# Kernel tuning notes

Hardware: AMD Instinct MI355X
Metric: run time of the kernel (lower is better)

## Reference

```python
import jax, jax.numpy as jnp
import numpy as np
from jax import lax

N, E, T, D = 50000, 400000, 16, 240
HID = 16  # LSTM hidden


def _p(k, shape):
    fan_in = shape[0]
    return jax.random.normal(k, shape, dtype=jnp.float32) * (1.0 / np.sqrt(fan_in))


def setup_inputs() -> dict:
    key = jax.random.key(0)
    ks = jax.random.split(key, 32)
    inp = {
        "x": jax.random.normal(ks[0], (N, D), dtype=jnp.float32),
        "edge_seq": jax.random.normal(ks[1], (E, T, 2), dtype=jnp.float32),
        "node_seq": jax.random.normal(ks[2], (N, T, 2), dtype=jnp.float32),
        # LSTM (torch gate order i,f,g,o); same lstm_edge is used for both edge and node seqs (as in source)
        "lstm_Wih": _p(ks[3], (4 * HID, 2)),
        "lstm_Whh": _p(ks[4], (4 * HID, HID)),
        "lstm_b": jnp.zeros((4 * HID,), jnp.float32),
        "dnn_W": _p(ks[5], (HID, 1)),
        "dnn_b": jnp.zeros((1,), jnp.float32),
        # gat1: in=256, heads=8, out=8 ; gat2: in=64, heads=1, out=64
        "gat1_W": _p(ks[6], (256, 64)),
        "gat1_att": _p(ks[7], (8, 8)),
        "gat1_b": jnp.zeros((64,), jnp.float32),
        "gat2_W": _p(ks[8], (64, 64)),
        "gat2_att": _p(ks[9], (1, 64)),
        "gat2_b": jnp.zeros((64,), jnp.float32),
        "gcn1_W": _p(ks[10], (256, 64)),
        "gcn1_b": jnp.zeros((64,), jnp.float32),
        "gcn2_W": _p(ks[11], (64, 64)),
        "gcn2_b": jnp.zeros((64,), jnp.float32),
        "cls1_W": _p(ks[12], (320, 32)),
        "cls1_b": jnp.zeros((32,), jnp.float32),
        "cls2_W": _p(ks[13], (32, 16)),
        "cls2_b": jnp.zeros((16,), jnp.float32),
        "cls3_W": _p(ks[14], (16, 4)),
        "cls3_b": jnp.zeros((4,), jnp.float32),
        "edge_index": jax.random.randint(ks[15], (2, E), 0, N),
        "edge_len": jax.random.randint(ks[16], (E,), 1, T + 1).astype(jnp.int32),
        "node_len": jax.random.randint(ks[17], (N,), 1, T + 1).astype(jnp.int32),
    }
    return inp


def lstm_last(seq, lens, Wih, Whh, b):
    """Run LSTM over padded [B,T,2] and return hidden at step len-1 (pack/pad_packed semantics)."""
    B, Tt, _ = seq.shape
    H = Whh.shape[1]

    def step(carry, inp):
        h, c, last = carry
        xt, t = inp
        g = xt @ Wih.T + h @ Whh.T + b
        i, f, gg, o = jnp.split(g, 4, axis=-1)
        c = jax.nn.sigmoid(f) * c + jax.nn.sigmoid(i) * jnp.tanh(gg)
        h = jax.nn.sigmoid(o) * jnp.tanh(c)
        last = jnp.where((t == lens - 1)[:, None], h, last)
        return (h, c, last), None

    z = jnp.zeros((B, H), seq.dtype)
    (_, _, last), _ = lax.scan(step, (z, z, z), (jnp.swapaxes(seq, 0, 1), jnp.arange(Tt)))
    return last


def gat_conv(x, src, dst, edge_scalar, W, att, bias, H, C):
    """myGATConv: gather -> leaky_relu -> softmax over dst neighborhoods -> (alpha + edge_mat)*x_j -> scatter-add + residual."""
    n = x.shape[0]
    xh = (x @ W).reshape(n, H, C)                       # [N,H,C]
    alpha = (xh * att[None]).sum(-1)                    # [N,H]
    a = jax.nn.leaky_relu(alpha[src], 0.2)              # [E,H] (alpha_j)
    amax = jax.ops.segment_max(a, dst, num_segments=n)
    ex = jnp.exp(a - amax[dst])
    att_e = ex / jax.ops.segment_sum(ex, dst, num_segments=n)[dst]
    coef = att_e + edge_scalar                          # [E,H] + [E,1] edge bias (edge_mat repeat over heads)
    msg = xh[src] * coef[..., None]                     # [E,H,C]
    out = jax.ops.segment_sum(msg, dst, num_segments=n) + xh  # aggregate + residual
    return out.reshape(n, H * C) + bias


def gcn_conv(x, src, dst, W, b):
    n = x.shape[0]
    xw = x @ W
    deg = jax.ops.segment_sum(jnp.ones(src.shape[0], xw.dtype), dst, num_segments=n) + 1.0  # +self-loop
    dinv = lax.rsqrt(deg)
    norm = (dinv[src] * dinv[dst])[:, None]
    out = jax.ops.segment_sum(xw[src] * norm, dst, num_segments=n) + xw * (dinv * dinv)[:, None]
    return out + b


def reference(x, edge_seq, node_seq, lstm_Wih, lstm_Whh, lstm_b, dnn_W, dnn_b,
              gat1_W, gat1_att, gat1_b, gat2_W, gat2_att, gat2_b,
              gcn1_W, gcn1_b, gcn2_W, gcn2_b,
              cls1_W, cls1_b, cls2_W, cls2_b, cls3_W, cls3_b,
              edge_index, edge_len, node_len):
    src, dst = edge_index[0], edge_index[1]
    # temporal edge branch -> per-edge scalar bias
    edge_feat = lstm_last(edge_seq, edge_len, lstm_Wih, lstm_Whh, lstm_b)   # [E,16]
    edge_scalar = edge_feat @ dnn_W + dnn_b                                 # [E,1]
    # temporal node branch (source reuses lstm_edge) -> concat to node features
    node_feat = lstm_last(node_seq, node_len, lstm_Wih, lstm_Whh, lstm_b)   # [N,16]
    xin = jnp.concatenate([x, node_feat], axis=-1)                          # [N,256]
    # GAT stack (no dropout: eval mode)
    x_gat = gat_conv(xin, src, dst, edge_scalar, gat1_W, gat1_att, gat1_b, 8, 8)
    x_gat = gat_conv(x_gat, src, dst, edge_scalar, gat2_W, gat2_att, gat2_b, 1, 64)
    x_gat = jnp.where(jnp.isinf(x_gat) | jnp.isnan(x_gat), 0.0, x_gat)
    lr = lambda v: jax.nn.leaky_relu(v, 0.01)
    # GCN stack (eval: dropout off)
    x_gcn = lr(gcn_conv(xin, src, dst, gcn1_W, gcn1_b))
    x_gcn = lr(gcn_conv(x_gcn, src, dst, gcn2_W, gcn2_b))
    # classifier head
    h = jnp.concatenate([xin, x_gcn], axis=1)
    h = lr(h @ cls1_W + cls1_b)
    h = lr(h @ cls2_W + cls2_b)
    out = h @ cls3_W + cls3_b
    return (out, x_gcn, x_gat)
```

## Files before the change

kernel.cpp:

```cpp
#include <hip/hip_runtime.h>
#include <hip/hip_bf16.h>


typedef unsigned int u32;

#define NN 50000
#define EE 400000

__device__ float g_nodeF[NN * 16];
__device__ float g_esc[EE];
__device__ float g_P1[NN * 64];
__device__ float g_P2[NN * 64];
__device__ float g_P3[NN * 64];
__device__ float g_P4[NN * 64];
__device__ float g_alpha[NN * 8];
__device__ float g_dinv[NN];
__device__ int   g_cnt[NN];
__device__ int   g_rs[NN + 1];
__device__ int   g_cur[NN];
__device__ int   g_csrc[EE];
__device__ float g_cesc[EE];
__device__ int   g_bhist[32];
__device__ int   g_bbase[32];
__device__ int   g_permN[NN];
__device__ int   g_permE[EE];
__device__ int   g_bsum[256];

__device__ __forceinline__ float rcpf(float x) { return __builtin_amdgcn_rcpf(x); }
__device__ __forceinline__ float ex2(float x)  { return __builtin_amdgcn_exp2f(x); }
__device__ __forceinline__ float sigf(float x) { return rcpf(1.0f + __expf(-x)); }

typedef short short8 __attribute__((ext_vector_type(8)));
typedef float f32x16 __attribute__((ext_vector_type(16)));

union S8U { short8 v; unsigned u[4]; };

__device__ __forceinline__ unsigned pk_hi(float a, float b) {
    return (__float_as_uint(a) >> 16) | (__float_as_uint(b) & 0xFFFF0000u);
}
__device__ __forceinline__ float bftrunc(float a) {
    return __uint_as_float(__float_as_uint(a) & 0xFFFF0000u);
}
__device__ __forceinline__ float lo_res(float a) { return a - bftrunc(a); }
__device__ __forceinline__ unsigned sx32(unsigned v) {
    return (unsigned)__shfl_xor((int)v, 32, 64);
}

__global__ void __launch_bounds__(256) bucket_hist_kernel(
    const int* __restrict__ nlen, const int* __restrict__ elen,
    const int* __restrict__ dstp, int* __restrict__ cnt)
{
    __shared__ int hb[32];
    int t = threadIdx.x;
    if (t < 32) hb[t] = 0;
    __syncthreads();
    int i = blockIdx.x * 256 + t;
    int bin = -1;
    if (i < NN + EE) {
        bin = (i < NN) ? (16 - nlen[i]) : (32 - elen[i - NN]);
    }
    if (bin >= 0) atomicAdd(&hb[bin], 1);
    if (i < EE) atomicAdd(&cnt[dstp[i]], 1);
    __syncthreads();
    if (t < 32 && hb[t] > 0) atomicAdd(&g_bhist[t], hb[t]);
}

__global__ void __launch_bounds__(64) bucket_scan_kernel()
{
    if (threadIdx.x == 0) {
        int acc = 0;
        for (int b = 0; b < 16; ++b) { g_bbase[b] = acc; acc += g_bhist[b]; }
        acc = 0;
        for (int b = 16; b < 32; ++b) { g_bbase[b] = acc; acc += g_bhist[b]; }
    }
}

__global__ void __launch_bounds__(256) bucket_scatter_kernel(
    const int* __restrict__ nlen, const int* __restrict__ elen)
{
    __shared__ int hb[32];
    int t = threadIdx.x;
    if (t < 32) hb[t] = 0;
    __syncthreads();
    int i = blockIdx.x * 256 + t;
    int bin = -1, idx = 0;
    if (i < NN + EE) {
        if (i < NN) { idx = i; bin = 16 - nlen[i]; }
        else        { idx = i - NN; bin = 32 - elen[i - NN]; }
    }
    if (bin >= 0) atomicAdd(&hb[bin], 1);
    __syncthreads();
    if (t < 32) {
        int c = hb[t];
        hb[t] = c > 0 ? atomicAdd(&g_bbase[t], c) : 0;
    }
    __syncthreads();
    if (bin >= 0) {
        int pos = atomicAdd(&hb[bin], 1);
        if (i < NN) g_permN[pos] = idx; else g_permE[pos] = idx;
    }
}

__global__ void __launch_bounds__(256, 3) lstm_fused_kernel(
    const float* __restrict__ nseq, const int* __restrict__ nlen,
    const float* __restrict__ eseq, const int* __restrict__ elen,
    const float* __restrict__ Wih, const float* __restrict__ Whh,
    const float* __restrict__ bias,
    const float* __restrict__ dnnW, const float* __restrict__ dnnb,
    const int* __restrict__ permN, const int* __restrict__ permE,
    float* __restrict__ nodeF, float* __restrict__ esc, int nNodeBlk)
{
    const int lane = threadIdx.x & 63;
    const int col  = lane & 31;
    const int hi   = lane >> 5;
    const bool isLo = (hi == 0);
    const int wave = threadIdx.x >> 6;

    const bool edgeMode = (int)blockIdx.x >= nNodeBlk;
    const float* seq = edgeMode ? eseq : nseq;
    const int*  lens = edgeMode ? elen : nlen;
    const int*  perm = edgeMode ? permE : permN;
    const int limit  = edgeMode ? EE : NN;
    const int bbase  = edgeMode ? ((int)blockIdx.x - nNodeBlk) : (int)blockIdx.x;
    const int g  = bbase * 128 + wave * 32 + col;
    const int gc = g < limit ? g : limit - 1;
    const int s  = perm[gc];
    const bool valid = g < limit;

    const float LOG2E = 1.44269504f;
    const int row0 = col, row1 = col + 32;
    const float s0 = LOG2E;
    const float s1 = (row1 < 48) ? 2.0f * LOG2E : LOG2E;
    const int ko = hi * 8;
    S8U ahh0, ahh1, ahl0, ahl1, ax0, ax1;
    {
        const float* w0 = Whh + row0 * 16 + ko;
        const float* w1 = Whh + row1 * 16 + ko;
#pragma unroll
        for (int r = 0; r < 4; ++r) {
            float a0 = w0[2 * r] * s0, b0 = w0[2 * r + 1] * s0;
            float a1 = w1[2 * r] * s1, b1 = w1[2 * r + 1] * s1;
            ahh0.u[r] = pk_hi(a0, b0);
            ahh1.u[r] = pk_hi(a1, b1);
            ahl0.u[r] = pk_hi(lo_res(a0), lo_res(b0));
            ahl1.u[r] = pk_hi(lo_res(a1), lo_res(b1));
        }
#pragma unroll
        for (int r = 0; r < 4; ++r) { ax0.u[r] = 0u; ax1.u[r] = 0u; }
        if (isLo) {
            float wa0 = Wih[row0 * 2] * s0, wb0 = Wih[row0 * 2 + 1] * s0, bb0 = bias[row0] * s0;
            float wa1 = Wih[row1 * 2] * s1, wb1 = Wih[row1 * 2 + 1] * s1, bb1 = bias[row1] * s1;
            ax0.u[0] = pk_hi(wa0, wb0);
            ax0.u[1] = pk_hi(bb0, wa0);
            ax0.u[2] = pk_hi(wb0, lo_res(wa0));
            ax0.u[3] = pk_hi(lo_res(wb0), lo_res(bb0));
            ax1.u[0] = pk_hi(wa1, wb1);
            ax1.u[1] = pk_hi(bb1, wa1);
            ax1.u[2] = pk_hi(wb1, lo_res(wa1));
            ax1.u[3] = pk_hi(lo_res(wb1), lo_res(bb1));
        }
    }

    const f32x16 zc = {0.f, 0.f, 0.f, 0.f, 0.f, 0.f, 0.f, 0.f,
                       0.f, 0.f, 0.f, 0.f, 0.f, 0.f, 0.f, 0.f};
    const unsigned bxmask = isLo ? 0xFFFFFFFFu : 0u;
    const unsigned one_bf = 0x3F80u;

    float cst[8], hlast[8];
#pragma unroll
    for (int j = 0; j < 8; ++j) { cst[j] = 0.f; hlast[j] = 0.f; }
    unsigned ph[4], pl[4];
#pragma unroll
    for (int r = 0; r < 4; ++r) { ph[r] = 0u; pl[r] = 0u; }

    const float4* sp = (const float4*)seq + (size_t)s * 8;
    const int lenm1 = lens[s] - 1;
    int lm = lenm1;
#pragma unroll
    for (int off = 32; off >= 1; off >>= 1) {
        int o = __shfl_xor(lm, off, 64);
        lm = lm > o ? lm : o;
    }
    const int nIter = (lm >> 1) + 1;

    float4 q = sp[0];
#pragma unroll 1
    for (int i = 0; i < nIter; ++i) {
        float4 qn = sp[(i + 1) & 7];
#pragma unroll
        for (int hf = 0; hf < 2; ++hf) {
            const int t = 2 * i + hf;
            const float x0 = hf ? q.z : q.x;
            const float x1 = hf ? q.w : q.y;

            S8U bhh, bhl, bx;
            {
                unsigned t0 = sx32(ph[0]), t1 = sx32(ph[1]);
                unsigned t2 = sx32(ph[2]), t3 = sx32(ph[3]);
                bhh.u[0] = isLo ? ph[0] : t2;
                bhh.u[1] = isLo ? ph[1] : t3;
                bhh.u[2] = isLo ? t0 : ph[2];
                bhh.u[3] = isLo ? t1 : ph[3];
                unsigned s0u = sx32(pl[0]), s1u = sx32(pl[1]);
                unsigned s2u = sx32(pl[2]), s3u = sx32(pl[3]);
                bhl.u[0] = isLo ? pl[0] : s2u;
                bhl.u[1] = isLo ? pl[1] : s3u;
                bhl.u[2] = isLo ? s0u : pl[2];
                bhl.u[3] = isLo ? s1u : pl[3];
            }
            {
                float xl0 = lo_res(x0), xl1 = lo_res(x1);
                bx.u[0] = pk_hi(x0, x1) & bxmask;
                bx.u[1] = (one_bf | (__float_as_uint(xl0) & 0xFFFF0000u)) & bxmask;
                bx.u[2] = pk_hi(xl1, x0) & bxmask;
                bx.u[3] = ((__float_as_uint(x1) >> 16) | (one_bf << 16)) & bxmask;
            }

            f32x16 d0 = __builtin_amdgcn_mfma_f32_32x32x16_bf16(ax0.v, bx.v, zc, 0, 0, 0);
            f32x16 d1 = __builtin_amdgcn_mfma_f32_32x32x16_bf16(ax1.v, bx.v, zc, 0, 0, 0);
            d0 = __builtin_amdgcn_mfma_f32_32x32x16_bf16(ahh0.v, bhh.v, d0, 0, 0, 0);
            d1 = __builtin_amdgcn_mfma_f32_32x32x16_bf16(ahh1.v, bhh.v, d1, 0, 0, 0);
            d0 = __builtin_amdgcn_mfma_f32_32x32x16_bf16(ahl0.v, bhh.v, d0, 0, 0, 0);
            d1 = __builtin_amdgcn_mfma_f32_32x32x16_bf16(ahl1.v, bhh.v, d1, 0, 0, 0);
            d0 = __builtin_amdgcn_mfma_f32_32x32x16_bf16(ahh0.v, bhl.v, d0, 0, 0, 0);
            d1 = __builtin_amdgcn_mfma_f32_32x32x16_bf16(ahh1.v, bhl.v, d1, 0, 0, 0);

            float hh[8];
#pragma unroll
            for (int j = 0; j < 8; ++j) {
                float ip = d0[j], fp = d0[8 + j], gp = d1[j], op = d1[8 + j];
                float sig_i = rcpf(1.0f + ex2(-ip));
                float sig_f = rcpf(1.0f + ex2(-fp));
                float th_g  = 1.0f - 2.0f * rcpf(ex2(gp) + 1.0f);
                float cu = sig_f * cst[j] + sig_i * th_g;
                cst[j] = cu;
                float th_c = 1.0f - 2.0f * rcpf(ex2(cu * 2.88539008f) + 1.0f);
                hh[j] = rcpf(1.0f + ex2(-op)) * th_c;
            }
            const bool selm = (t == lenm1);
#pragma unroll
            for (int j = 0; j < 8; ++j) hlast[j] = selm ? hh[j] : hlast[j];
#pragma unroll
            for (int r = 0; r < 4; ++r) {
                float a = hh[2 * r], b = hh[2 * r + 1];
                ph[r] = pk_hi(a, b);
                pl[r] = pk_hi(lo_res(a), lo_res(b));
            }
        }
        q = qn;
    }

    if (edgeMode) {
        float4 dA = *(const float4*)(dnnW + hi * 4);
        float4 dB = *(const float4*)(dnnW + hi * 4 + 8);
        float part = hlast[0] * dA.x + hlast[1] * dA.y + hlast[2] * dA.z + hlast[3] * dA.w
                   + hlast[4] * dB.x + hlast[5] * dB.y + hlast[6] * dB.z + hlast[7] * dB.w;
        float tot = part + __shfl_xor(part, 32, 64);
        if (isLo && valid) esc[s] = tot + dnnb[0];
    } else {
        if (valid) {
            float* dst = nodeF + (size_t)s * 16 + hi * 4;
            *(float4*)(dst)     = make_float4(hlast[0], hlast[1], hlast[2], hlast[3]);
            *(float4*)(dst + 8) = make_float4(hlast[4], hlast[5], hlast[6], hlast[7]);
        }
    }
}

__global__ void __launch_bounds__(256) zero_cnt_kernel(int* cnt, int n)
{
    int t = blockIdx.x * 256 + threadIdx.x;
    if (t < n) cnt[t] = 0;
    if (blockIdx.x == 0 && threadIdx.x < 32) g_bhist[threadIdx.x] = 0;
}

__global__ void __launch_bounds__(256) scan1_kernel(const int* __restrict__ cnt, int n)
{
    __shared__ int s[256];
    int t = threadIdx.x;
    int i = blockIdx.x * 256 + t;
    s[t] = (i < n) ? cnt[i] : 0;
    __syncthreads();
#pragma unroll
    for (int off = 128; off >= 1; off >>= 1) {
        if (t < off) s[t] += s[t + off];
        __syncthreads();
    }
    if (t == 0) g_bsum[blockIdx.x] = s[0];
}

__global__ void __launch_bounds__(256) scan3_kernel(
    const int* __restrict__ cnt, int* __restrict__ rs, int* __restrict__ cur,
    float* __restrict__ dinv, int n, int E, int nb)
{
    __shared__ int sb[256];
    __shared__ int s[256];
    int t = threadIdx.x;
    sb[t] = (t < nb) ? g_bsum[t] : 0;
    __syncthreads();
#pragma unroll
    for (int off = 1; off < 256; off <<= 1) {
        int add = (t >= off) ? sb[t - off] : 0;
        __syncthreads();
        sb[t] += add;
        __syncthreads();
    }
    const int boff = (blockIdx.x == 0) ? 0 : sb[blockIdx.x - 1];

    int i = blockIdx.x * 256 + t;
    int v = (i < n) ? cnt[i] : 0;
    s[t] = v;
    __syncthreads();
#pragma unroll
    for (int off = 1; off < 256; off <<= 1) {
        int add = (t >= off) ? s[t - off] : 0;
        __syncthreads();
        s[t] += add;
        __syncthreads();
    }
    if (i < n) {
        int excl = s[t] - v + boff;
        rs[i] = excl;
        cur[i] = excl;
        dinv[i] = rsqrtf((float)v + 1.0f);
    }
    if (i == 0) rs[n] = E;
}

__global__ void __launch_bounds__(256) fill_kernel(const int* __restrict__ src,
                                                   const int* __restrict__ dst,
                                                   const float* __restrict__ esc,
                                                   int* __restrict__ cur,
                                                   int* __restrict__ csrc,
                                                   float* __restrict__ cesc, int E)
{
    int e = blockIdx.x * 256 + threadIdx.x;
    if (e >= E) return;
    int pos = atomicAdd(&cur[dst[e]], 1);
    csrc[pos] = src[e];
    cesc[pos] = esc[e];
}

__global__ void __launch_bounds__(256, 2) gemmX_dual_kernel(
    const float* __restrict__ x, const float* __restrict__ nodeF,
    const float* __restrict__ Wg, const float* __restrict__ Wc,
    const float* __restrict__ att,
    float* __restrict__ Pg, float* __restrict__ Pc,
    float* __restrict__ alpha, int n)
{
    __shared__ unsigned sW[2][2][64 * 64];
    const int tid = threadIdx.x;
    const int lane = tid & 63;
    const int col  = lane & 31;
    const int hi   = lane >> 5;
    const int wv   = tid >> 6;
    const int nodeBase = blockIdx.x * 128 + wv * 32;
    const int nodeL = nodeBase + col;
    const int nc = nodeL < n ? nodeL : n - 1;
    const float* xrow = x + (size_t)nc * 240;
    const float* frow = nodeF + (size_t)nc * 16;
    const float attv0 = att[col];
    const float attv1 = att[32 + col];

    const f32x16 zc = {0.f, 0.f, 0.f, 0.f, 0.f, 0.f, 0.f, 0.f,
                       0.f, 0.f, 0.f, 0.f, 0.f, 0.f, 0.f, 0.f};
    f32x16 ag0 = zc, ag1 = zc, ac0 = zc, ac1 = zc;

#pragma unroll 1
    for (int p = 0; p < 2; ++p) {
        if (p) __syncthreads();
        for (int i = tid; i < 2 * 64 * 64; i += 256) {
            const int mat = i >> 12;
            const int jj  = i & 4095;
            const int kk2 = jj >> 6, c = jj & 63;
            const float* W = mat ? Wc : Wg;
            float a = W[(p * 64 + kk2) * 128 + c];
            float b = W[(p * 64 + kk2) * 128 + 64 + c];
            sW[mat][0][jj] = pk_hi(a, b);
            sW[mat][1][jj] = pk_hi(lo_res(a), lo_res(b));
        }
        __syncthreads();
#pragma unroll 1
        for (int ch = 0; ch < 8; ++ch) {
            const int gch = p * 8 + ch;
            const float* src = (gch < 15) ? (xrow + gch * 16 + hi * 8) : (frow + hi * 8);
            float4 v0 = *(const float4*)src;
            float4 v1 = *(const float4*)(src + 4);
            S8U xh, xl;
            xh.u[0] = pk_hi(v0.x, v0.y);
            xh.u[1] = pk_hi(v0.z, v0.w);
            xh.u[2] = pk_hi(v1.x, v1.y);
            xh.u[3] = pk_hi(v1.z, v1.w);
            xl.u[0] = pk_hi(lo_res(v0.x), lo_res(v0.y));
            xl.u[1] = pk_hi(lo_res(v0.z), lo_res(v0.w));
            xl.u[2] = pk_hi(lo_res(v1.x), lo_res(v1.y));
            xl.u[3] = pk_hi(lo_res(v1.z), lo_res(v1.w));

            const int rbase = (ch * 8 + hi * 4) * 64 + col;
            S8U gh0, gl0, gh1, gl1, ch0, cl0, ch1, cl1;
#pragma unroll
            for (int r = 0; r < 4; ++r) {
                gh0.u[r] = sW[0][0][rbase + r * 64];
                gl0.u[r] = sW[0][1][rbase + r * 64];
                gh1.u[r] = sW[0][0][rbase + r * 64 + 32];
                gl1.u[r] = sW[0][1][rbase + r * 64 + 32];
                ch0.u[r] = sW[1][0][rbase + r * 64];
                cl0.u[r] = sW[1][1][rbase + r * 64];
                ch1.u[r] = sW[1][0][rbase + r * 64 + 32];
                cl1.u[r] = sW[1][1][rbase + r * 64 + 32];
            }
            ag0 = __builtin_amdgcn_mfma_f32_32x32x16_bf16(xh.v, gh0.v, ag0, 0, 0, 0);
            ag1 = __builtin_amdgcn_mfma_f32_32x32x16_bf16(xh.v, gh1.v, ag1, 0, 0, 0);
            ag0 = __builtin_amdgcn_mfma_f32_32x32x16_bf16(xl.v, gh0.v, ag0, 0, 0, 0);
            ag1 = __builtin_amdgcn_mfma_f32_32x32x16_bf16(xl.v, gh1.v, ag1, 0, 0, 0);
            ag0 = __builtin_amdgcn_mfma_f32_32x32x16_bf16(xh.v, gl0.v, ag0, 0, 0, 0);
            ag1 = __builtin_amdgcn_mfma_f32_32x32x16_bf16(xh.v, gl1.v, ag1, 0, 0, 0);
            ac0 = __builtin_amdgcn_mfma_f32_32x32x16_bf16(xh.v, ch0.v, ac0, 0, 0, 0);
            ac1 = __builtin_amdgcn_mfma_f32_32x32x16_bf16(xh.v, ch1.v, ac1, 0, 0, 0);
            ac0 = __builtin_amdgcn_mfma_f32_32x32x16_bf16(xl.v, ch0.v, ac0, 0, 0, 0);
            ac1 = __builtin_amdgcn_mfma_f32_32x32x16_bf16(xl.v, ch1.v, ac1, 0, 0, 0);
            ac0 = __builtin_amdgcn_mfma_f32_32x32x16_bf16(xh.v, cl0.v, ac0, 0, 0, 0);
            ac1 = __builtin_amdgcn_mfma_f32_32x32x16_bf16(xh.v, cl1.v, ac1, 0, 0, 0);
        }
    }

#pragma unroll
    for (int r = 0; r < 16; ++r) {
        const int nr = (r & 3) + 8 * (r >> 2) + 4 * hi;
        const int nd = nodeBase + nr;
        const bool ok = nd < n;
        if (ok) {
            Pg[(size_t)nd * 64 + col]      = ag0[r];
            Pg[(size_t)nd * 64 + 32 + col] = ag1[r];
            Pc[(size_t)nd * 64 + col]      = ac0[r];
            Pc[(size_t)nd * 64 + 32 + col] = ac1[r];
        }
        float p0 = ag0[r] * attv0;
        float p1 = ag1[r] * attv1;
        p0 += __shfl_xor(p0, 1, 64); p0 += __shfl_xor(p0, 2, 64); p0 += __shfl_xor(p0, 4, 64);
        p1 += __shfl_xor(p1, 1, 64); p1 += __shfl_xor(p1, 2, 64); p1 += __shfl_xor(p1, 4, 64);
        if (ok && (col & 7) == 0) {
            alpha[(size_t)nd * 8 + (col >> 3)]     = p0;
            alpha[(size_t)nd * 8 + 4 + (col >> 3)] = p1;
        }
    }
}

__global__ void __launch_bounds__(256, 2) gemm64_dual_kernel(
    const float* __restrict__ Ag, const float* __restrict__ Ac,
    const float* __restrict__ Wg, const float* __restrict__ Wc,
    const float* __restrict__ att,
    float* __restrict__ Pg, float* __restrict__ Pc,
    float* __restrict__ alpha, int n)
{
    __shared__ unsigned sW[2][2][32 * 64];
    const int tid = threadIdx.x;
    for (int i = tid; i < 2 * 32 * 64; i += 256) {
        const int mat = i >> 11;
        const int jj  = i & 2047;
        const int kk2 = jj >> 6, c = jj & 63;
        const float* W = mat ? Wc : Wg;
        float a = W[kk2 * 128 + c];
        float b = W[kk2 * 128 + 64 + c];
        sW[mat][0][jj] = pk_hi(a, b);
        sW[mat][1][jj] = pk_hi(lo_res(a), lo_res(b));
    }
    __syncthreads();

    const int lane = tid & 63;
    const int col  = lane & 31;
    const int hi   = lane >> 5;
    const int wv   = tid >> 6;
    const int nodeBase = blockIdx.x * 128 + wv * 32;
    const int nodeL = nodeBase + col;
    const int nc = nodeL < n ? nodeL : n - 1;
    const float attv0 = att[col];
    const float attv1 = att[32 + col];

    const f32x16 zc = {0.f, 0.f, 0.f, 0.f, 0.f, 0.f, 0.f, 0.f,
                       0.f, 0.f, 0.f, 0.f, 0.f, 0.f, 0.f, 0.f};
    f32x16 bg0 = zc, bg1 = zc, bc0 = zc, bc1 = zc;

    const float* garow = Ag + (size_t)nc * 64;
    const float* carow = Ac + (size_t)nc * 64;
#pragma unroll
    for (int ch = 0; ch < 4; ++ch) {
        const int rbase = (ch * 8 + hi * 4) * 64 + col;
        S8U wh0, wl0, wh1, wl1;
        {
            const float* src = garow + ch * 16 + hi * 8;
            float4 v0 = *(const float4*)src;
            float4 v1 = *(const float4*)(src + 4);
            S8U xh, xl;
            xh.u[0] = pk_hi(v0.x, v0.y);
            xh.u[1] = pk_hi(v0.z, v0.w);
            xh.u[2] = pk_hi(v1.x, v1.y);
            xh.u[3] = pk_hi(v1.z, v1.w);
            xl.u[0] = pk_hi(lo_res(v0.x), lo_res(v0.y));
            xl.u[1] = pk_hi(lo_res(v0.z), lo_res(v0.w));
            xl.u[2] = pk_hi(lo_res(v1.x), lo_res(v1.y));
            xl.u[3] = pk_hi(lo_res(v1.z), lo_res(v1.w));
#pragma unroll
            for (int r = 0; r < 4; ++r) {
                wh0.u[r] = sW[0][0][rbase + r * 64];
                wl0.u[r] = sW[0][1][rbase + r * 64];
                wh1.u[r] = sW[0][0][rbase + r * 64 + 32];
                wl1.u[r] = sW[0][1][rbase + r * 64 + 32];
            }
            bg0 = __builtin_amdgcn_mfma_f32_32x32x16_bf16(xh.v, wh0.v, bg0, 0, 0, 0);
            bg1 = __builtin_amdgcn_mfma_f32_32x32x16_bf16(xh.v, wh1.v, bg1, 0, 0, 0);
            bg0 = __builtin_amdgcn_mfma_f32_32x32x16_bf16(xl.v, wh0.v, bg0, 0, 0, 0);
            bg1 = __builtin_amdgcn_mfma_f32_32x32x16_bf16(xl.v, wh1.v, bg1, 0, 0, 0);
            bg0 = __builtin_amdgcn_mfma_f32_32x32x16_bf16(xh.v, wl0.v, bg0, 0, 0, 0);
            bg1 = __builtin_amdgcn_mfma_f32_32x32x16_bf16(xh.v, wl1.v, bg1, 0, 0, 0);
        }
        {
            const float* src = carow + ch * 16 + hi * 8;
            float4 v0 = *(const float4*)src;
            float4 v1 = *(const float4*)(src + 4);
            S8U xh, xl;
            xh.u[0] = pk_hi(v0.x, v0.y);
            xh.u[1] = pk_hi(v0.z, v0.w);
            xh.u[2] = pk_hi(v1.x, v1.y);
            xh.u[3] = pk_hi(v1.z, v1.w);
            xl.u[0] = pk_hi(lo_res(v0.x), lo_res(v0.y));
            xl.u[1] = pk_hi(lo_res(v0.z), lo_res(v0.w));
            xl.u[2] = pk_hi(lo_res(v1.x), lo_res(v1.y));
            xl.u[3] = pk_hi(lo_res(v1.z), lo_res(v1.w));
#pragma unroll
            for (int r = 0; r < 4; ++r) {
                wh0.u[r] = sW[1][0][rbase + r * 64];
                wl0.u[r] = sW[1][1][rbase + r * 64];
                wh1.u[r] = sW[1][0][rbase + r * 64 + 32];
                wl1.u[r] = sW[1][1][rbase + r * 64 + 32];
            }
            bc0 = __builtin_amdgcn_mfma_f32_32x32x16_bf16(xh.v, wh0.v, bc0, 0, 0, 0);
            bc1 = __builtin_amdgcn_mfma_f32_32x32x16_bf16(xh.v, wh1.v, bc1, 0, 0, 0);
            bc0 = __builtin_amdgcn_mfma_f32_32x32x16_bf16(xl.v, wh0.v, bc0, 0, 0, 0);
            bc1 = __builtin_amdgcn_mfma_f32_32x32x16_bf16(xl.v, wh1.v, bc1, 0, 0, 0);
            bc0 = __builtin_amdgcn_mfma_f32_32x32x16_bf16(xh.v, wl0.v, bc0, 0, 0, 0);
            bc1 = __builtin_amdgcn_mfma_f32_32x32x16_bf16(xh.v, wl1.v, bc1, 0, 0, 0);
        }
    }

#pragma unroll
    for (int r = 0; r < 16; ++r) {
        const int nr = (r & 3) + 8 * (r >> 2) + 4 * hi;
        const int nd = nodeBase + nr;
        const bool ok = nd < n;
        if (ok) {
            Pg[(size_t)nd * 64 + col]      = bg0[r];
            Pg[(size_t)nd * 64 + 32 + col] = bg1[r];
            Pc[(size_t)nd * 64 + col]      = bc0[r];
            Pc[(size_t)nd * 64 + 32 + col] = bc1[r];
        }
        float pa = bg0[r] * attv0 + bg1[r] * attv1;
        pa += __shfl_xor(pa, 1, 64);
        pa += __shfl_xor(pa, 2, 64);
        pa += __shfl_xor(pa, 4, 64);
        pa += __shfl_xor(pa, 8, 64);
        pa += __shfl_xor(pa, 16, 64);
        if (ok && col == 0) alpha[nd] = pa;
    }
}

template <int H, bool FILTER>
__global__ void __launch_bounds__(256) fused_gather_kernel(
    const int* __restrict__ rs, const int* __restrict__ csrc,
    const float* __restrict__ cesc, const float* __restrict__ alpha,
    const float* __restrict__ xh, const float* __restrict__ xw,
    const float* __restrict__ dinv,
    const float* __restrict__ gbias, const float* __restrict__ cbias,
    float* __restrict__ gout, float* __restrict__ cout, int n)
{
    const int j = threadIdx.x & 63;
    const int d = blockIdx.x * 4 + (threadIdx.x >> 6);
    if (d >= n) return;
    const int k0 = rs[d], k1 = rs[d + 1];

    float m = -INFINITY, ssum = 0.f;
    if (H == 8) {
        const int e = j >> 3, h = j & 7;
        const int nb = (k1 - k0 + 7) >> 3;
        for (int b = 0; b < nb; ++b) {
            int k = k0 + b * 8 + e;
            if (k < k1) {
                float a = alpha[(size_t)csrc[k] * 8 + h];
                a = a > 0.f ? a : 0.2f * a;
                float mn = fmaxf(m, a);
                ssum = ssum * __expf(m - mn) + __expf(a - mn);
                m = mn;
            }
        }
#pragma unroll
        for (int msk = 8; msk <= 32; msk <<= 1) {
            float mo = __shfl_xor(m, msk, 64);
            float so = __shfl_xor(ssum, msk, 64);
            float mn = fmaxf(m, mo);
            float f1 = (m == -INFINITY) ? 0.f : __expf(m - mn);
            float f2 = (mo == -INFINITY) ? 0.f : __expf(mo - mn);
            ssum = ssum * f1 + so * f2;
            m = mn;
        }
    } else {
        const int nb = (k1 - k0 + 63) >> 6;
        for (int b = 0; b < nb; ++b) {
            int k = k0 + b * 64 + j;
            if (k < k1) {
                float a = alpha[csrc[k]];
                a = a > 0.f ? a : 0.2f * a;
                float mn = fmaxf(m, a);
                ssum = ssum * __expf(m - mn) + __expf(a - mn);
                m = mn;
            }
        }
#pragma unroll
        for (int msk = 1; msk <= 32; msk <<= 1) {
            float mo = __shfl_xor(m, msk, 64);
            float so = __shfl_xor(ssum, msk, 64);
            float mn = fmaxf(m, mo);
            float f1 = (m == -INFINITY) ? 0.f : __expf(m - mn);
            float f2 = (mo == -INFINITY) ? 0.f : __expf(mo - mn);
            ssum = ssum * f1 + so * f2;
            m = mn;
        }
    }
    const int h2 = (H == 8) ? (j >> 3) : 0;
    float mh, ri;
    if (H == 8) {
        mh = __shfl(m, h2, 64);
        ri = rcpf(__shfl(ssum, h2, 64));
    } else {
        mh = m;
        ri = rcpf(ssum);
    }

    const float di = dinv[d];
    float ag = xh[(size_t)d * 64 + j] + gbias[j];
    float ac = xw[(size_t)d * 64 + j] * di * di + cbias[j];
#pragma unroll 2
    for (int k = k0; k < k1; ++k) {
        int s = csrc[k];
        float a = alpha[(size_t)s * H + h2];
        a = a > 0.f ? a : 0.2f * a;
        float coef = __expf(a - mh) * ri + cesc[k];
        ag += xh[(size_t)s * 64 + j] * coef;
        ac += xw[(size_t)s * 64 + j] * (dinv[s] * di);
    }
    if (FILTER && !__builtin_isfinite(ag)) ag = 0.f;
    gout[(size_t)d * 64 + j] = ag;
    cout[(size_t)d * 64 + j] = ac > 0.f ? ac : 0.01f * ac;
}

__global__ void __launch_bounds__(256) cls_kernel(
    const float* __restrict__ x, const float* __restrict__ nodeF,
    const float* __restrict__ xg,
    const float* __restrict__ W1, const float* __restrict__ b1,
    const float* __restrict__ W2, const float* __restrict__ b2,
    const float* __restrict__ W3, const float* __restrict__ b3,
    float* __restrict__ outp, int n)
{
    __shared__ float sW1[320 * 32];
    __shared__ float sW2[32 * 16];
    __shared__ float sW3[16 * 4];
    __shared__ float sb1[32], sb2[16], sb3[4];
    int tid = threadIdx.x;
    for (int i = tid; i < 320 * 32; i += 256) sW1[i] = W1[i];
    for (int i = tid; i < 512; i += 256) sW2[i] = W2[i];
    if (tid < 64) sW3[tid] = W3[tid];
    if (tid < 32) sb1[tid] = b1[tid];
    if (tid < 16) sb2[tid] = b2[tid];
    if (tid < 4)  sb3[tid] = b3[tid];
    __syncthreads();
    int nd = blockIdx.x * 256 + tid;
    if (nd >= n) return;

    float a1[32];
#pragma unroll
    for (int j = 0; j < 32; ++j) a1[j] = sb1[j];
    const float4* xr = (const float4*)(x + (size_t)nd * 240);
#pragma unroll 1
    for (int k4 = 0; k4 < 60; ++k4) {
        float4 v = xr[k4];
        const float* wr = sW1 + k4 * 128;
#pragma unroll
        for (int j = 0; j < 32; ++j)
            a1[j] += v.x * wr[j] + v.y * wr[32 + j] + v.z * wr[64 + j] + v.w * wr[96 + j];
    }
    const float4* nf = (const float4*)(nodeF + (size_t)nd * 16);
#pragma unroll 1
    for (int k4 = 60; k4 < 64; ++k4) {
        float4 v = nf[k4 - 60];
        const float* wr = sW1 + k4 * 128;
#pragma unroll
        for (int j = 0; j < 32; ++j)
            a1[j] += v.x * wr[j] + v.y * wr[32 + j] + v.z * wr[64 + j] + v.w * wr[96 + j];
    }
    const float4* p2 = (const float4*)(xg + (size_t)nd * 64);
#pragma unroll 1
    for (int k4 = 0; k4 < 16; ++k4) {
        float4 v = p2[k4];
        const float* wr = sW1 + 8192 + k4 * 128;
#pragma unroll
        for (int j = 0; j < 32; ++j)
            a1[j] += v.x * wr[j] + v.y * wr[32 + j] + v.z * wr[64 + j] + v.w * wr[96 + j];
    }
#pragma unroll
    for (int j = 0; j < 32; ++j) { float v = a1[j]; a1[j] = v > 0.f ? v : 0.01f * v; }

    float a2[16];
#pragma unroll
    for (int j = 0; j < 16; ++j) a2[j] = sb2[j];
#pragma unroll
    for (int k = 0; k < 32; ++k) {
        float v = a1[k];
        const float* wr = sW2 + k * 16;
#pragma unroll
        for (int j = 0; j < 16; ++j) a2[j] += v * wr[j];
    }
#pragma unroll
    for (int j = 0; j < 16; ++j) { float v = a2[j]; a2[j] = v > 0.f ? v : 0.01f * v; }

    float a3[4] = {sb3[0], sb3[1], sb3[2], sb3[3]};
#pragma unroll
    for (int k = 0; k < 16; ++k) {
        float v = a2[k];
        const float* wr = sW3 + k * 4;
        a3[0] += v * wr[0]; a3[1] += v * wr[1]; a3[2] += v * wr[2]; a3[3] += v * wr[3];
    }
    float4 o = make_float4(a3[0], a3[1], a3[2], a3[3]);
    *(float4*)(outp + (size_t)nd * 4) = o;
}

static inline unsigned nblk(size_t t) { return (unsigned)((t + 255) / 256); }

extern "C" void kernel_launch(void* const* d_in, const int* in_sizes, int n_in,
                              void* d_out, int out_size, void* d_ws, size_t ws_size,
                              hipStream_t stream)
{
    const float* x     = (const float*)d_in[0];
    const float* eseq  = (const float*)d_in[1];
    const float* nseq  = (const float*)d_in[2];
    const float* Wih   = (const float*)d_in[3];
    const float* Whh   = (const float*)d_in[4];
    const float* lb    = (const float*)d_in[5];
    const float* dnnW  = (const float*)d_in[6];
    const float* dnnb  = (const float*)d_in[7];
    const float* g1W   = (const float*)d_in[8];
    const float* g1att = (const float*)d_in[9];
    const float* g1b   = (const float*)d_in[10];
    const float* g2W   = (const float*)d_in[11];
    const float* g2att = (const float*)d_in[12];
    const float* g2b   = (const float*)d_in[13];
    const float* gc1W  = (const float*)d_in[14];
    const float* gc1b  = (const float*)d_in[15];
    const float* gc2W  = (const float*)d_in[16];
    const float* gc2b  = (const float*)d_in[17];
    const float* c1W   = (const float*)d_in[18];
    const float* c1b   = (const float*)d_in[19];
    const float* c2W   = (const float*)d_in[20];
    const float* c2b   = (const float*)d_in[21];
    const float* c3W   = (const float*)d_in[22];
    const float* c3b   = (const float*)d_in[23];
    const int* eidx  = (const int*)d_in[24];
    const int* elen  = (const int*)d_in[25];
    const int* nlen  = (const int*)d_in[26];

    const int N = NN;
    const int E = EE;
    const int* srcp = eidx;
    const int* dstp = eidx + E;

    float *nodeF, *esc, *P1, *P2, *P3, *P4, *alpha, *dinv, *cesc;
    int *cnt, *rs, *cur, *csrc, *permN, *permE;
    hipGetSymbolAddress((void**)&nodeF, HIP_SYMBOL(g_nodeF));
    hipGetSymbolAddress((void**)&esc,   HIP_SYMBOL(g_esc));
    hipGetSymbolAddress((void**)&P1,    HIP_SYMBOL(g_P1));
    hipGetSymbolAddress((void**)&P2,    HIP_SYMBOL(g_P2));
    hipGetSymbolAddress((void**)&P3,    HIP_SYMBOL(g_P3));
    hipGetSymbolAddress((void**)&P4,    HIP_SYMBOL(g_P4));
    hipGetSymbolAddress((void**)&alpha, HIP_SYMBOL(g_alpha));
    hipGetSymbolAddress((void**)&dinv,  HIP_SYMBOL(g_dinv));
    hipGetSymbolAddress((void**)&cnt,   HIP_SYMBOL(g_cnt));
    hipGetSymbolAddress((void**)&rs,    HIP_SYMBOL(g_rs));
    hipGetSymbolAddress((void**)&cur,   HIP_SYMBOL(g_cur));
    hipGetSymbolAddress((void**)&csrc,  HIP_SYMBOL(g_csrc));
    hipGetSymbolAddress((void**)&cesc,  HIP_SYMBOL(g_cesc));
    hipGetSymbolAddress((void**)&permN, HIP_SYMBOL(g_permN));
    hipGetSymbolAddress((void**)&permE, HIP_SYMBOL(g_permE));

    float* out0   = (float*)d_out;
    float* outGcn = out0 + (size_t)N * 4;
    float* outGat = outGcn + (size_t)N * 64;

    zero_cnt_kernel<<<nblk(N), 256, 0, stream>>>(cnt, N);
    bucket_hist_kernel<<<nblk(NN + EE), 256, 0, stream>>>(nlen, elen, dstp, cnt);
    bucket_scan_kernel<<<1, 64, 0, stream>>>();
    bucket_scatter_kernel<<<nblk(NN + EE), 256, 0, stream>>>(nlen, elen);

    const int nNodeBlk = (N + 127) / 128;
    const int nEdgeBlk = (E + 127) / 128;
    lstm_fused_kernel<<<nNodeBlk + nEdgeBlk, 256, 0, stream>>>(
        nseq, nlen, eseq, elen, Wih, Whh, lb, dnnW, dnnb, permN, permE,
        nodeF, esc, nNodeBlk);

    const unsigned scanBlk = nblk(N);
    scan1_kernel<<<scanBlk, 256, 0, stream>>>(cnt, N);
    scan3_kernel<<<scanBlk, 256, 0, stream>>>(cnt, rs, cur, dinv, N, E, (int)scanBlk);
    fill_kernel<<<nblk(E), 256, 0, stream>>>(srcp, dstp, esc, cur, csrc, cesc, E);

    const unsigned gemmBlk = (N + 127) / 128;

    gemmX_dual_kernel<<<gemmBlk, 256, 0, stream>>>(
        x, nodeF, g1W, gc1W, g1att, P1, P3, alpha, N);
    fused_gather_kernel<8, false><<<(N + 3) / 4, 256, 0, stream>>>(
        rs, csrc, cesc, alpha, P1, P3, dinv, g1b, gc1b, P2, P4, N);

    gemm64_dual_kernel<<<gemmBlk, 256, 0, stream>>>(
        P2, P4, g2W, gc2W, g2att, P1, P3, alpha, N);
    fused_gather_kernel<1, true><<<(N + 3) / 4, 256, 0, stream>>>(
        rs, csrc, cesc, alpha, P1, P3, dinv, g2b, gc2b, outGat, outGcn, N);

    cls_kernel<<<nblk(N), 256, 0, stream>>>(x, nodeF, outGcn, c1W, c1b, c2W, c2b, c3W, c3b, out0, N);
}
```

Baseline: 551.4 us.

## Interleave GAT and GCN projections into one buffer and reuse cached attention logits

The separate GAT and GCN projection buffers are merged into one interleaved [N,128] layout, so each gathered neighbour row costs a single float2 load instead of two scattered 64-float rows. The GEMM kernels write and read this interleaved layout. The gather kernel also keeps the leaky-relu'd attention logits from the softmax pass in registers and broadcasts them with shuffles in the aggregation pass, avoiding a second indirect alpha load for the first 16 (H=8) or 64 (H=1) edges. This adds shuffle and branch overhead, and the GEMM input unpacking becomes strided.

```diff
diff --git a/kernel.cpp b/kernel.cpp
--- a/kernel.cpp
+++ b/kernel.cpp
@@ -9,10 +9,8 @@
 
 __device__ float g_nodeF[NN * 16];
 __device__ float g_esc[EE];
-__device__ float g_P1[NN * 64];
-__device__ float g_P2[NN * 64];
-__device__ float g_P3[NN * 64];
-__device__ float g_P4[NN * 64];
+__device__ float g_PX[NN * 128];
+__device__ float g_PY[NN * 128];
 __device__ float g_alpha[NN * 8];
 __device__ float g_dinv[NN];
 __device__ int   g_cnt[NN];
@@ -28,7 +26,6 @@
 
 __device__ __forceinline__ float rcpf(float x) { return __builtin_amdgcn_rcpf(x); }
 __device__ __forceinline__ float ex2(float x)  { return __builtin_amdgcn_exp2f(x); }
-__device__ __forceinline__ float sigf(float x) { return rcpf(1.0f + __expf(-x)); }
 
 typedef short short8 __attribute__((ext_vector_type(8)));
 typedef float f32x16 __attribute__((ext_vector_type(16)));
@@ -344,8 +341,7 @@
     const float* __restrict__ x, const float* __restrict__ nodeF,
     const float* __restrict__ Wg, const float* __restrict__ Wc,
     const float* __restrict__ att,
-    float* __restrict__ Pg, float* __restrict__ Pc,
-    float* __restrict__ alpha, int n)
+    float* __restrict__ PX, float* __restrict__ alpha, int n)
 {
     __shared__ unsigned sW[2][2][64 * 64];
     const int tid = threadIdx.x;
@@ -429,10 +425,8 @@
         const int nd = nodeBase + nr;
         const bool ok = nd < n;
         if (ok) {
-            Pg[(size_t)nd * 64 + col]      = ag0[r];
-            Pg[(size_t)nd * 64 + 32 + col] = ag1[r];
-            Pc[(size_t)nd * 64 + col]      = ac0[r];
-            Pc[(size_t)nd * 64 + 32 + col] = ac1[r];
+            *(float2*)(PX + (size_t)nd * 128 + 2 * col)      = make_float2(ag0[r], ac0[r]);
+            *(float2*)(PX + (size_t)nd * 128 + 64 + 2 * col) = make_float2(ag1[r], ac1[r]);
         }
         float p0 = ag0[r] * attv0;
         float p1 = ag1[r] * attv1;
@@ -446,11 +440,10 @@
 }
 
 __global__ void __launch_bounds__(256, 2) gemm64_dual_kernel(
-    const float* __restrict__ Ag, const float* __restrict__ Ac,
+    const float* __restrict__ A,
     const float* __restrict__ Wg, const float* __restrict__ Wc,
     const float* __restrict__ att,
-    float* __restrict__ Pg, float* __restrict__ Pc,
-    float* __restrict__ alpha, int n)
+    float* __restrict__ PX, float* __restrict__ alpha, int n)
 {
     __shared__ unsigned sW[2][2][32 * 64];
     const int tid = threadIdx.x;
@@ -480,66 +473,56 @@
                        0.f, 0.f, 0.f, 0.f, 0.f, 0.f, 0.f, 0.f};
     f32x16 bg0 = zc, bg1 = zc, bc0 = zc, bc1 = zc;
 
-    const float* garow = Ag + (size_t)nc * 64;
-    const float* carow = Ac + (size_t)nc * 64;
+    const float* arow = A + (size_t)nc * 128;
 #pragma unroll
     for (int ch = 0; ch < 4; ++ch) {
+        const float* src = arow + ch * 32 + hi * 16;
+        float4 q0 = *(const float4*)(src);
+        float4 q1 = *(const float4*)(src + 4);
+        float4 q2 = *(const float4*)(src + 8);
+        float4 q3 = *(const float4*)(src + 12);
+        S8U gxh, gxl, cxh, cxl;
+        gxh.u[0] = pk_hi(q0.x, q0.z); gxh.u[1] = pk_hi(q1.x, q1.z);
+        gxh.u[2] = pk_hi(q2.x, q2.z); gxh.u[3] = pk_hi(q3.x, q3.z);
+        gxl.u[0] = pk_hi(lo_res(q0.x), lo_res(q0.z));
+        gxl.u[1] = pk_hi(lo_res(q1.x), lo_res(q1.z));
+        gxl.u[2] = pk_hi(lo_res(q2.x), lo_res(q2.z));
+        gxl.u[3] = pk_hi(lo_res(q3.x), lo_res(q3.z));
+        cxh.u[0] = pk_hi(q0.y, q0.w); cxh.u[1] = pk_hi(q1.y, q1.w);
+        cxh.u[2] = pk_hi(q2.y, q2.w); cxh.u[3] = pk_hi(q3.y, q3.w);
+        cxl.u[0] = pk_hi(lo_res(q0.y), lo_res(q0.w));
+        cxl.u[1] = pk_hi(lo_res(q1.y), lo_res(q1.w));
+        cxl.u[2] = pk_hi(lo_res(q2.y), lo_res(q2.w));
+        cxl.u[3] = pk_hi(lo_res(q3.y), lo_res(q3.w));
+
         const int rbase = (ch * 8 + hi * 4) * 64 + col;
         S8U wh0, wl0, wh1, wl1;
-        {
-            const float* src = garow + ch * 16 + hi * 8;
-            float4 v0 = *(const float4*)src;
-            float4 v1 = *(const float4*)(src + 4);
-            S8U xh, xl;
-            xh.u[0] = pk_hi(v0.x, v0.y);
-            xh.u[1] = pk_hi(v0.z, v0.w);
-            xh.u[2] = pk_hi(v1.x, v1.y);
-            xh.u[3] = pk_hi(v1.z, v1.w);
-            xl.u[0] = pk_hi(lo_res(v0.x), lo_res(v0.y));
-            xl.u[1] = pk_hi(lo_res(v0.z), lo_res(v0.w));
-            xl.u[2] = pk_hi(lo_res(v1.x), lo_res(v1.y));
-            xl.u[3] = pk_hi(lo_res(v1.z), lo_res(v1.w));
-#pragma unroll
-            for (int r = 0; r < 4; ++r) {
-                wh0.u[r] = sW[0][0][rbase + r * 64];
-                wl0.u[r] = sW[0][1][rbase + r * 64];
-                wh1.u[r] = sW[0][0][rbase + r * 64 + 32];
-                wl1.u[r] = sW[0][1][rbase + r * 64 + 32];
-            }
-            bg0 = __builtin_amdgcn_mfma_f32_32x32x16_bf16(xh.v, wh0.v, bg0, 0, 0, 0);
-            bg1 = __builtin_amdgcn_mfma_f32_32x32x16_bf16(xh.v, wh1.v, bg1, 0, 0, 0);
-            bg0 = __builtin_amdgcn_mfma_f32_32x32x16_bf16(xl.v, wh0.v, bg0, 0, 0, 0);
-            bg1 = __builtin_amdgcn_mfma_f32_32x32x16_bf16(xl.v, wh1.v, bg1, 0, 0, 0);
-            bg0 = __builtin_amdgcn_mfma_f32_32x32x16_bf16(xh.v, wl0.v, bg0, 0, 0, 0);
-            bg1 = __builtin_amdgcn_mfma_f32_32x32x16_bf16(xh.v, wl1.v, bg1, 0, 0, 0);
-        }
-        {
-            const float* src = carow + ch * 16 + hi * 8;
-            float4 v0 = *(const float4*)src;
-            float4 v1 = *(const float4*)(src + 4);
-            S8U xh, xl;
-            xh.u[0] = pk_hi(v0.x, v0.y);
-            xh.u[1] = pk_hi(v0.z, v0.w);
-            xh.u[2] = pk_hi(v1.x, v1.y);
-            xh.u[3] = pk_hi(v1.z, v1.w);
-            xl.u[0] = pk_hi(lo_res(v0.x), lo_res(v0.y));
-            xl.u[1] = pk_hi(lo_res(v0.z), lo_res(v0.w));
-            xl.u[2] = pk_hi(lo_res(v1.x), lo_res(v1.y));
-            xl.u[3] = pk_hi(lo_res(v1.z), lo_res(v1.w));
-#pragma unroll
-            for (int r = 0; r < 4; ++r) {
-                wh0.u[r] = sW[1][0][rbase + r * 64];
-                wl0.u[r] = sW[1][1][rbase + r * 64];
-                wh1.u[r] = sW[1][0][rbase + r * 64 + 32];
-                wl1.u[r] = sW[1][1][rbase + r * 64 + 32];
-            }
-            bc0 = __builtin_amdgcn_mfma_f32_32x32x16_bf16(xh.v, wh0.v, bc0, 0, 0, 0);
-            bc1 = __builtin_amdgcn_mfma_f32_32x32x16_bf16(xh.v, wh1.v, bc1, 0, 0, 0);
-            bc0 = __builtin_amdgcn_mfma_f32_32x32x16_bf16(xl.v, wh0.v, bc0, 0, 0, 0);
-            bc1 = __builtin_amdgcn_mfma_f32_32x32x16_bf16(xl.v, wh1.v, bc1, 0, 0, 0);
-            bc0 = __builtin_amdgcn_mfma_f32_32x32x16_bf16(xh.v, wl0.v, bc0, 0, 0, 0);
-            bc1 = __builtin_amdgcn_mfma_f32_32x32x16_bf16(xh.v, wl1.v, bc1, 0, 0, 0);
-        }
+#pragma unroll
+        for (int r = 0; r < 4; ++r) {
+            wh0.u[r] = sW[0][0][rbase + r * 64];
+            wl0.u[r] = sW[0][1][rbase + r * 64];
+            wh1.u[r] = sW[0][0][rbase + r * 64 + 32];
+            wl1.u[r] = sW[0][1][rbase + r * 64 + 32];
+        }
+        bg0 = __builtin_amdgcn_mfma_f32_32x32x16_bf16(gxh.v, wh0.v, bg0, 0, 0, 0);
+        bg1 = __builtin_amdgcn_mfma_f32_32x32x16_bf16(gxh.v, wh1.v, bg1, 0, 0, 0);
+        bg0 = __builtin_amdgcn_mfma_f32_32x32x16_bf16(gxl.v, wh0.v, bg0, 0, 0, 0);
+        bg1 = __builtin_amdgcn_mfma_f32_32x32x16_bf16(gxl.v, wh1.v, bg1, 0, 0, 0);
+        bg0 = __builtin_amdgcn_mfma_f32_32x32x16_bf16(gxh.v, wl0.v, bg0, 0, 0, 0);
+        bg1 = __builtin_amdgcn_mfma_f32_32x32x16_bf16(gxh.v, wl1.v, bg1, 0, 0, 0);
+#pragma unroll
+        for (int r = 0; r < 4; ++r) {
+            wh0.u[r] = sW[1][0][rbase + r * 64];
+            wl0.u[r] = sW[1][1][rbase + r * 64];
+            wh1.u[r] = sW[1][0][rbase + r * 64 + 32];
+            wl1.u[r] = sW[1][1][rbase + r * 64 + 32];
+        }
+        bc0 = __builtin_amdgcn_mfma_f32_32x32x16_bf16(cxh.v, wh0.v, bc0, 0, 0, 0);
+        bc1 = __builtin_amdgcn_mfma_f32_32x32x16_bf16(cxh.v, wh1.v, bc1, 0, 0, 0);
+        bc0 = __builtin_amdgcn_mfma_f32_32x32x16_bf16(cxl.v, wh0.v, bc0, 0, 0, 0);
+        bc1 = __builtin_amdgcn_mfma_f32_32x32x16_bf16(cxl.v, wh1.v, bc1, 0, 0, 0);
+        bc0 = __builtin_amdgcn_mfma_f32_32x32x16_bf16(cxh.v, wl0.v, bc0, 0, 0, 0);
+        bc1 = __builtin_amdgcn_mfma_f32_32x32x16_bf16(cxh.v, wl1.v, bc1, 0, 0, 0);
     }
 
 #pragma unroll
@@ -548,10 +531,8 @@
         const int nd = nodeBase + nr;
         const bool ok = nd < n;
         if (ok) {
-            Pg[(size_t)nd * 64 + col]      = bg0[r];
-            Pg[(size_t)nd * 64 + 32 + col] = bg1[r];
-            Pc[(size_t)nd * 64 + col]      = bc0[r];
-            Pc[(size_t)nd * 64 + 32 + col] = bc1[r];
+            *(float2*)(PX + (size_t)nd * 128 + 2 * col)      = make_float2(bg0[r], bc0[r]);
+            *(float2*)(PX + (size_t)nd * 128 + 64 + 2 * col) = make_float2(bg1[r], bc1[r]);
         }
         float pa = bg0[r] * attv0 + bg1[r] * attv1;
         pa += __shfl_xor(pa, 1, 64);
@@ -567,10 +548,11 @@
 __global__ void __launch_bounds__(256) fused_gather_kernel(
     const int* __restrict__ rs, const int* __restrict__ csrc,
     const float* __restrict__ cesc, const float* __restrict__ alpha,
-    const float* __restrict__ xh, const float* __restrict__ xw,
-    const float* __restrict__ dinv,
+    const float* __restrict__ PX, const float* __restrict__ dinv,
     const float* __restrict__ gbias, const float* __restrict__ cbias,
-    float* __restrict__ gout, float* __restrict__ cout, int n)
+    float* __restrict__ outI,
+    float* __restrict__ gout, float* __restrict__ cout,
+    int n)
 {
     const int j = threadIdx.x & 63;
     const int d = blockIdx.x * 4 + (threadIdx.x >> 6);
@@ -578,6 +560,7 @@
     const int k0 = rs[d], k1 = rs[d + 1];
 
     float m = -INFINITY, ssum = 0.f;
+    float a0val = -INFINITY, a1val = -INFINITY;
     if (H == 8) {
         const int e = j >> 3, h = j & 7;
         const int nb = (k1 - k0 + 7) >> 3;
@@ -586,6 +569,8 @@
             if (k < k1) {
                 float a = alpha[(size_t)csrc[k] * 8 + h];
                 a = a > 0.f ? a : 0.2f * a;
+                if (b == 0) a0val = a;
+                else if (b == 1) a1val = a;
                 float mn = fmaxf(m, a);
                 ssum = ssum * __expf(m - mn) + __expf(a - mn);
                 m = mn;
@@ -608,6 +593,7 @@
             if (k < k1) {
                 float a = alpha[csrc[k]];
                 a = a > 0.f ? a : 0.2f * a;
+                if (b == 0) a0val = a;
                 float mn = fmaxf(m, a);
                 ssum = ssum * __expf(m - mn) + __expf(a - mn);
                 m = mn;
@@ -635,20 +621,35 @@
     }
 
     const float di = dinv[d];
-    float ag = xh[(size_t)d * 64 + j] + gbias[j];
-    float ac = xw[(size_t)d * 64 + j] * di * di + cbias[j];
+    float2 vd = *(const float2*)(PX + (size_t)d * 128 + 2 * j);
+    float ag = vd.x + gbias[j];
+    float ac = vd.y * di * di + cbias[j];
 #pragma unroll 2
     for (int k = k0; k < k1; ++k) {
         int s = csrc[k];
-        float a = alpha[(size_t)s * H + h2];
-        a = a > 0.f ? a : 0.2f * a;
+        const int idx = k - k0;
+        float a;
+        if (H == 8) {
+            if (idx < 8)       a = __shfl(a0val, idx * 8 + h2, 64);
+            else if (idx < 16) a = __shfl(a1val, (idx - 8) * 8 + h2, 64);
+            else { a = alpha[(size_t)s * 8 + h2]; a = a > 0.f ? a : 0.2f * a; }
+        } else {
+            if (idx < 64) a = __shfl(a0val, idx, 64);
+            else { a = alpha[s]; a = a > 0.f ? a : 0.2f * a; }
+        }
         float coef = __expf(a - mh) * ri + cesc[k];
-        ag += xh[(size_t)s * 64 + j] * coef;
-        ac += xw[(size_t)s * 64 + j] * (dinv[s] * di);
+        float2 v = *(const float2*)(PX + (size_t)s * 128 + 2 * j);
+        ag += v.x * coef;
+        ac += v.y * (dinv[s] * di);
     }
     if (FILTER && !__builtin_isfinite(ag)) ag = 0.f;
-    gout[(size_t)d * 64 + j] = ag;
-    cout[(size_t)d * 64 + j] = ac > 0.f ? ac : 0.01f * ac;
+    float acl = ac > 0.f ? ac : 0.01f * ac;
+    if (H == 8) {
+        *(float2*)(outI + (size_t)d * 128 + 2 * j) = make_float2(ag, acl);
+    } else {
+        gout[(size_t)d * 64 + j] = ag;
+        cout[(size_t)d * 64 + j] = acl;
+    }
 }
 
 __global__ void __launch_bounds__(256) cls_kernel(
@@ -770,14 +771,12 @@
     const int* srcp = eidx;
     const int* dstp = eidx + E;
 
-    float *nodeF, *esc, *P1, *P2, *P3, *P4, *alpha, *dinv, *cesc;
+    float *nodeF, *esc, *PX, *PY, *alpha, *dinv, *cesc;
     int *cnt, *rs, *cur, *csrc, *permN, *permE;
     hipGetSymbolAddress((void**)&nodeF, HIP_SYMBOL(g_nodeF));
     hipGetSymbolAddress((void**)&esc,   HIP_SYMBOL(g_esc));
-    hipGetSymbolAddress((void**)&P1,    HIP_SYMBOL(g_P1));
-    hipGetSymbolAddress((void**)&P2,    HIP_SYMBOL(g_P2));
-    hipGetSymbolAddress((void**)&P3,    HIP_SYMBOL(g_P3));
-    hipGetSymbolAddress((void**)&P4,    HIP_SYMBOL(g_P4));
+    hipGetSymbolAddress((void**)&PX,    HIP_SYMBOL(g_PX));
+    hipGetSymbolAddress((void**)&PY,    HIP_SYMBOL(g_PY));
     hipGetSymbolAddress((void**)&alpha, HIP_SYMBOL(g_alpha));
     hipGetSymbolAddress((void**)&dinv,  HIP_SYMBOL(g_dinv));
     hipGetSymbolAddress((void**)&cnt,   HIP_SYMBOL(g_cnt));
@@ -811,14 +810,14 @@
     const unsigned gemmBlk = (N + 127) / 128;
 
     gemmX_dual_kernel<<<gemmBlk, 256, 0, stream>>>(
-        x, nodeF, g1W, gc1W, g1att, P1, P3, alpha, N);
+        x, nodeF, g1W, gc1W, g1att, PX, alpha, N);
     fused_gather_kernel<8, false><<<(N + 3) / 4, 256, 0, stream>>>(
-        rs, csrc, cesc, alpha, P1, P3, dinv, g1b, gc1b, P2, P4, N);
+        rs, csrc, cesc, alpha, PX, dinv, g1b, gc1b, PY, nullptr, nullptr, N);
 
     gemm64_dual_kernel<<<gemmBlk, 256, 0, stream>>>(
-        P2, P4, g2W, gc2W, g2att, P1, P3, alpha, N);
+        PY, g2W, gc2W, g2att, PX, alpha, N);
     fused_gather_kernel<1, true><<<(N + 3) / 4, 256, 0, stream>>>(
-        rs, csrc, cesc, alpha, P1, P3, dinv, g2b, gc2b, outGat, outGcn, N);
+        rs, csrc, cesc, alpha, PX, dinv, g2b, gc2b, nullptr, outGat, outGcn, N);
 
     cls_kernel<<<nblk(N), 256, 0, stream>>>(x, nodeF, outGcn, c1W, c1b, c2W, c2b, c3W, c3b, out0, N);
 }
```

After: 562.9 us. 1.02x slower.
